# Kernel tuning notes

Measured on AMD Instinct MI355X. Metric: run time of the kernel, lower is better.

## Reference

```python
import jax, jax.numpy as jnp
import numpy as np

NUM_EXPERTS = 8
TOP_K = 2
HIDDEN = 1024
NUM_TOKENS = 8192


def setup_inputs() -> dict:
    key = jax.random.key(0)
    k1, k2, k3 = jax.random.split(key, 3)
    x = jax.random.normal(k1, (NUM_TOKENS, HIDDEN), dtype=jnp.float32)
    # gate: nn.Linear(hidden, num_experts, bias=False) -> weight [E, H]
    gate_w = jax.random.normal(k2, (NUM_EXPERTS, HIDDEN), dtype=jnp.float32) * 0.02
    # experts: nn.Linear(hidden, hidden, bias=False) stacked -> [E, H_out, H_in]
    expert_w = jax.random.normal(k3, (NUM_EXPERTS, HIDDEN, HIDDEN), dtype=jnp.float32) * 0.02
    return {"x": x, "gate_w": gate_w, "expert_w": expert_w}


def reference(x, gate_w, expert_w):
    # --- routing ---
    logits = jnp.einsum("th,eh->te", x, gate_w)          # [T, E]
    probs = jax.nn.softmax(logits, axis=-1)
    weights, indices = jax.lax.top_k(probs, TOP_K)        # [T, K], [T, K]

    # --- expert compute (equivalent of dispatch + per-expert GEMM) ---
    # y_e = x @ W_e^T for every expert; tokens then gather their top-k rows.
    all_y = jnp.einsum("td,ehd->eth", x, expert_w)        # [E, T, H]

    # --- weighted combine (gather by routed expert ids) ---
    t_idx = jnp.arange(x.shape[0])[None, :]               # [1, T]
    y_sel = all_y[indices.T, t_idx, :]                    # [K, T, H]
    out = jnp.einsum("tk,kth->th", weights, y_sel)        # [T, H]
    return out
```

## Files before the change

### kernel.cpp

```cpp
#include <hip/hip_runtime.h>
#include <hip/hip_bf16.h>
#include <stdint.h>

#define NUM_TOKENS 8192
#define HIDDEN 1024
#define NEXP 8
#define TOPK 2

typedef __bf16 bf16;
typedef __bf16 bf16x4 __attribute__((ext_vector_type(4)));
typedef __bf16 bf16x8 __attribute__((ext_vector_type(8)));
typedef float f32x4 __attribute__((ext_vector_type(4)));

__device__ __forceinline__ void gld_lds16(const void* g, void* l) {
  __builtin_amdgcn_global_load_lds(
      (const __attribute__((address_space(1))) void*)(uintptr_t)g,
      (__attribute__((address_space(3))) void*)(uint32_t)(uintptr_t)l,
      16, 0, 0);
}

__global__ __launch_bounds__(256) void gate_route_kernel(
    const float* __restrict__ x, const float* __restrict__ gw,
    bf16* __restrict__ xbf, int* __restrict__ echoice, float* __restrict__ pchoice)
{
  const int wid  = threadIdx.x >> 6;
  const int lane = threadIdx.x & 63;
  const int t = blockIdx.x * 4 + wid;

  const float* xrow = x + (size_t)t * HIDDEN;
  bf16* xbrow = xbf + (size_t)t * HIDDEN;

  float acc[NEXP];
#pragma unroll
  for (int e = 0; e < NEXP; ++e) acc[e] = 0.f;

#pragma unroll
  for (int it = 0; it < 4; ++it) {
    const int idx = it * 256 + lane * 4;
    float4 xv = *(const float4*)(xrow + idx);
    bf16x4 xb;
    xb[0] = (bf16)xv.x; xb[1] = (bf16)xv.y; xb[2] = (bf16)xv.z; xb[3] = (bf16)xv.w;
    *(bf16x4*)(xbrow + idx) = xb;
#pragma unroll
    for (int e = 0; e < NEXP; ++e) {
      float4 gv = *(const float4*)(gw + e * HIDDEN + idx);
      acc[e] += xv.x * gv.x + xv.y * gv.y + xv.z * gv.z + xv.w * gv.w;
    }
  }
#pragma unroll
  for (int e = 0; e < NEXP; ++e) {
#pragma unroll
    for (int off = 32; off > 0; off >>= 1)
      acc[e] += __shfl_xor(acc[e], off, 64);
  }

  if (lane == 0) {
    float m = acc[0];
#pragma unroll
    for (int e = 1; e < NEXP; ++e) m = fmaxf(m, acc[e]);
    float p[NEXP]; float s = 0.f;
#pragma unroll
    for (int e = 0; e < NEXP; ++e) { p[e] = expf(acc[e] - m); s += p[e]; }
    const float inv = 1.f / s;
#pragma unroll
    for (int e = 0; e < NEXP; ++e) p[e] *= inv;
    int i0 = 0; float p0 = p[0];
#pragma unroll
    for (int e = 1; e < NEXP; ++e) if (p[e] > p0) { p0 = p[e]; i0 = e; }
    int i1 = -1; float p1 = -1.f;
#pragma unroll
    for (int e = 0; e < NEXP; ++e) if (e != i0 && p[e] > p1) { p1 = p[e]; i1 = e; }

    echoice[t]              = i0;
    echoice[NUM_TOKENS + t] = i1;
    pchoice[t]              = p0;
    pchoice[NUM_TOKENS + t] = p1;
  }
}

__global__ __launch_bounds__(1024) void build_lists_kernel(
    const int* __restrict__ echoice, const float* __restrict__ pchoice,
    int* __restrict__ cnt, int* __restrict__ tok, float* __restrict__ wt)
{
  const int tid  = threadIdx.x;
  const int wave = tid >> 6;
  const int lane = tid & 63;
  const int k = wave >> 3;
  const int w = wave & 7;
  const int tbase = w * 1024;

  const int*   ec = echoice + k * NUM_TOKENS;
  const float* pc = pchoice + k * NUM_TOKENS;

  __shared__ int wcnt[2][8][NEXP];
  __shared__ int woff[2][8][NEXP];

  const unsigned long long lower = ((unsigned long long)1 << lane) - 1;

  int   ev[16];
  float pv[16];
#pragma unroll
  for (int c = 0; c < 16; ++c) {
    ev[c] = ec[tbase + c * 64 + lane];
    pv[c] = pc[tbase + c * 64 + lane];
  }

  int cl[NEXP];
#pragma unroll
  for (int e = 0; e < NEXP; ++e) cl[e] = 0;
#pragma unroll
  for (int c = 0; c < 16; ++c) {
#pragma unroll
    for (int l = 0; l < NEXP; ++l)
      cl[l] += __popcll(__ballot(ev[c] == l));
  }
  if (lane < NEXP) wcnt[k][w][lane] = cl[lane];
  __syncthreads();

  if (lane < NEXP) {
    int off = 0;
#pragma unroll
    for (int ww = 0; ww < 8; ++ww) {
      if (ww == w) woff[k][w][lane] = off;
      off += wcnt[k][ww][lane];
    }
    if (w == 0) cnt[k * NEXP + lane] = off;
  }
  __syncthreads();

  int run[NEXP];
#pragma unroll
  for (int e = 0; e < NEXP; ++e) run[e] = woff[k][w][e];
#pragma unroll
  for (int c = 0; c < 16; ++c) {
    const int e = ev[c];
    int pos = 0;
#pragma unroll
    for (int l = 0; l < NEXP; ++l) {
      const unsigned long long m = __ballot(ev[c] == l);
      if (e == l) pos = run[l] + __popcll(m & lower);
      run[l] += __popcll(m);
    }
    const int list = k * NEXP + e;
    tok[(size_t)list * NUM_TOKENS + pos] = tbase + c * 64 + lane;
    wt [(size_t)list * NUM_TOKENS + pos] = pv[c];
  }
}

__global__ __launch_bounds__(256) void convert_w_kernel(
    const float* __restrict__ w, bf16* __restrict__ wbf)
{
  const size_t i = ((size_t)blockIdx.x * 256 + threadIdx.x) * 4;
  float4 v = *(const float4*)(w + i);
  bf16x4 b;
  b[0] = (bf16)v.x; b[1] = (bf16)v.y; b[2] = (bf16)v.z; b[3] = (bf16)v.w;
  *(bf16x4*)(wbf + i) = b;
}

__global__ __launch_bounds__(256) void moe_gemm_kernel(
    const bf16* __restrict__ xbf, const bf16* __restrict__ wbf,
    const int* __restrict__ cnt, const int* __restrict__ tok,
    const float* __restrict__ wt, float* __restrict__ out)
{
  const int e  = blockIdx.z >> 1;
  const int k  = blockIdx.z & 1;
  const int list = k * NEXP + e;
  const int mt = blockIdx.y;
  const int nt = blockIdx.x;
  const int count = cnt[list];
  const int m0 = mt * 128;
  if (m0 >= count) return;
  const int rows = min(128, count - m0);

  __shared__ __align__(16) bf16 As[128 * 32];
  __shared__ __align__(16) bf16 Bs[128 * 32];
  __shared__ int   tok_s[128];
  __shared__ float wt_s[128];

  const int tid = threadIdx.x;
  if (tid < 128) {
    if (tid < rows) {
      tok_s[tid] = tok[(size_t)list * NUM_TOKENS + m0 + tid];
      wt_s[tid]  = wt [(size_t)list * NUM_TOKENS + m0 + tid];
    } else { tok_s[tid] = 0; wt_s[tid] = 0.f; }
  }
  __syncthreads();

  const int rr = tid >> 2;
  const int c8 = tid & 3;
  const bf16* gA0 = xbf + (size_t)tok_s[rr] * HIDDEN + c8 * 8;
  const bf16* gA1 = xbf + (size_t)tok_s[64 + rr] * HIDDEN + c8 * 8;
  const bf16* gB0 = wbf + (size_t)e * HIDDEN * HIDDEN
                  + (size_t)(nt * 128 + rr) * HIDDEN + c8 * 8;
  const bf16* gB1 = gB0 + (size_t)64 * HIDDEN;
  bf16* lA = As + tid * 8;
  bf16* lB = Bs + tid * 8;

  const int wid  = tid >> 6;
  const int lane = tid & 63;
  const int wm = (wid >> 1) * 64;
  const int wn = (wid & 1) * 64;
  const int qm = lane & 15;
  const int q8 = (lane >> 4) * 8;

  f32x4 acc[4][4];
#pragma unroll
  for (int i = 0; i < 4; ++i)
#pragma unroll
    for (int j = 0; j < 4; ++j) acc[i][j] = (f32x4){0.f, 0.f, 0.f, 0.f};

  for (int kc = 0; kc < HIDDEN; kc += 32) {
    gld_lds16(gA0 + kc, lA);
    gld_lds16(gA1 + kc, lA + 64 * 32);
    gld_lds16(gB0 + kc, lB);
    gld_lds16(gB1 + kc, lB + 64 * 32);
    __syncthreads();

    bf16x8 a[4], b[4];
#pragma unroll
    for (int i = 0; i < 4; ++i)
      a[i] = *(const bf16x8*)(As + (wm + i * 16 + qm) * 32 + q8);
#pragma unroll
    for (int j = 0; j < 4; ++j)
      b[j] = *(const bf16x8*)(Bs + (wn + j * 16 + qm) * 32 + q8);
#pragma unroll
    for (int i = 0; i < 4; ++i)
#pragma unroll
      for (int j = 0; j < 4; ++j)
        acc[i][j] = __builtin_amdgcn_mfma_f32_16x16x32_bf16(a[i], b[j], acc[i][j], 0, 0, 0);
    __syncthreads();
  }

  const int h0 = nt * 128 + wn + (lane & 15);
#pragma unroll
  for (int i = 0; i < 4; ++i) {
    const int rbase = wm + i * 16 + (lane >> 4) * 4;
#pragma unroll
    for (int r = 0; r < 4; ++r) {
      const int rl = rbase + r;
      if (rl < rows) {
        const int t = tok_s[rl];
        const float w = wt_s[rl];
        float* orow = out + (size_t)t * HIDDEN + h0;
#pragma unroll
        for (int j = 0; j < 4; ++j) {
          const float v = w * acc[i][j][r];
          unsafeAtomicAdd(orow + j * 16, v);
        }
      }
    }
  }
}

extern "C" void kernel_launch(void* const* d_in, const int* in_sizes, int n_in,
                              void* d_out, int out_size, void* d_ws, size_t ws_size,
                              hipStream_t stream) {
  const float* x  = (const float*)d_in[0];
  const float* gw = (const float*)d_in[1];
  const float* ew = (const float*)d_in[2];
  float* out = (float*)d_out;

  char* ws = (char*)d_ws;
  int*   cnt     = (int*)ws;
  int*   echoice = (int*)(ws + 256);
  float* pchoice = (float*)(ws + 256 + (size_t)2 * NUM_TOKENS * 4);
  int*   tok = (int*)(ws + 256 + (size_t)4 * NUM_TOKENS * 4);
  float* wt  = (float*)(ws + 256 + (size_t)20 * NUM_TOKENS * 4);
  bf16*  xbf = (bf16*)(ws + 256 + (size_t)36 * NUM_TOKENS * 4);
  bf16*  wbf = (bf16*)((char*)xbf + (size_t)NUM_TOKENS * HIDDEN * 2);

  hipMemsetAsync(out, 0, (size_t)NUM_TOKENS * HIDDEN * sizeof(float), stream);

  gate_route_kernel<<<NUM_TOKENS / 4, 256, 0, stream>>>(x, gw, xbf, echoice, pchoice);
  build_lists_kernel<<<1, 1024, 0, stream>>>(echoice, pchoice, cnt, tok, wt);
  convert_w_kernel<<<(NEXP * HIDDEN * HIDDEN) / (4 * 256), 256, 0, stream>>>(ew, wbf);

  dim3 grid(HIDDEN / 128, NUM_TOKENS / 128, 2 * NEXP);
  moe_gemm_kernel<<<grid, 256, 0, stream>>>(xbf, wbf, cnt, tok, wt, out);
}
```

Baseline: 233.0 us.

## Double-buffer MoE GEMM with K=64 swizzled LDS tiles and parallelize list building

```diff
diff --git a/kernel.cpp b/kernel.cpp
--- a/kernel.cpp
+++ b/kernel.cpp
@@ -82,68 +82,51 @@
     const int* __restrict__ echoice, const float* __restrict__ pchoice,
     int* __restrict__ cnt, int* __restrict__ tok, float* __restrict__ wt)
 {
+  const int list = blockIdx.x;
+  const int k = list >> 3;
+  const int e = list & 7;
   const int tid  = threadIdx.x;
   const int wave = tid >> 6;
   const int lane = tid & 63;
-  const int k = wave >> 3;
-  const int w = wave & 7;
-  const int tbase = w * 1024;
+  const int tbase = wave * 512;
 
   const int*   ec = echoice + k * NUM_TOKENS;
   const float* pc = pchoice + k * NUM_TOKENS;
 
-  __shared__ int wcnt[2][8][NEXP];
-  __shared__ int woff[2][8][NEXP];
+  __shared__ int wcnt[16];
+  __shared__ int woff[16];
 
   const unsigned long long lower = ((unsigned long long)1 << lane) - 1;
 
-  int   ev[16];
-  float pv[16];
-#pragma unroll
-  for (int c = 0; c < 16; ++c) {
+  int   ev[8];
+  float pv[8];
+#pragma unroll
+  for (int c = 0; c < 8; ++c) {
     ev[c] = ec[tbase + c * 64 + lane];
     pv[c] = pc[tbase + c * 64 + lane];
   }
-
-  int cl[NEXP];
-#pragma unroll
-  for (int e = 0; e < NEXP; ++e) cl[e] = 0;
-#pragma unroll
-  for (int c = 0; c < 16; ++c) {
-#pragma unroll
-    for (int l = 0; l < NEXP; ++l)
-      cl[l] += __popcll(__ballot(ev[c] == l));
-  }
-  if (lane < NEXP) wcnt[k][w][lane] = cl[lane];
-  __syncthreads();
-
-  if (lane < NEXP) {
+  unsigned long long m[8];
+  int cl = 0;
+#pragma unroll
+  for (int c = 0; c < 8; ++c) { m[c] = __ballot(ev[c] == e); cl += __popcll(m[c]); }
+  if (lane == 0) wcnt[wave] = cl;
+  __syncthreads();
+  if (tid == 0) {
     int off = 0;
 #pragma unroll
-    for (int ww = 0; ww < 8; ++ww) {
-      if (ww == w) woff[k][w][lane] = off;
-      off += wcnt[k][ww][lane];
-    }
-    if (w == 0) cnt[k * NEXP + lane] = off;
-  }
-  __syncthreads();
-
-  int run[NEXP];
-#pragma unroll
-  for (int e = 0; e < NEXP; ++e) run[e] = woff[k][w][e];
-#pragma unroll
-  for (int c = 0; c < 16; ++c) {
-    const int e = ev[c];
-    int pos = 0;
-#pragma unroll
-    for (int l = 0; l < NEXP; ++l) {
-      const unsigned long long m = __ballot(ev[c] == l);
-      if (e == l) pos = run[l] + __popcll(m & lower);
-      run[l] += __popcll(m);
-    }
-    const int list = k * NEXP + e;
-    tok[(size_t)list * NUM_TOKENS + pos] = tbase + c * 64 + lane;
-    wt [(size_t)list * NUM_TOKENS + pos] = pv[c];
+    for (int w = 0; w < 16; ++w) { woff[w] = off; off += wcnt[w]; }
+    cnt[list] = off;
+  }
+  __syncthreads();
+  int run = woff[wave];
+#pragma unroll
+  for (int c = 0; c < 8; ++c) {
+    if (ev[c] == e) {
+      const int pos = run + __popcll(m[c] & lower);
+      tok[(size_t)list * NUM_TOKENS + pos] = tbase + c * 64 + lane;
+      wt [(size_t)list * NUM_TOKENS + pos] = pv[c];
+    }
+    run += __popcll(m[c]);
   }
 }
 
@@ -172,8 +155,8 @@
   if (m0 >= count) return;
   const int rows = min(128, count - m0);
 
-  __shared__ __align__(16) bf16 As[128 * 32];
-  __shared__ __align__(16) bf16 Bs[128 * 32];
+  __shared__ __align__(16) bf16 As[2 * 128 * 64];
+  __shared__ __align__(16) bf16 Bs[2 * 128 * 64];
   __shared__ int   tok_s[128];
   __shared__ float wt_s[128];
 
@@ -186,22 +169,25 @@
   }
   __syncthreads();
 
-  const int rr = tid >> 2;
-  const int c8 = tid & 3;
-  const bf16* gA0 = xbf + (size_t)tok_s[rr] * HIDDEN + c8 * 8;
-  const bf16* gA1 = xbf + (size_t)tok_s[64 + rr] * HIDDEN + c8 * 8;
-  const bf16* gB0 = wbf + (size_t)e * HIDDEN * HIDDEN
-                  + (size_t)(nt * 128 + rr) * HIDDEN + c8 * 8;
-  const bf16* gB1 = gB0 + (size_t)64 * HIDDEN;
-  bf16* lA = As + tid * 8;
-  bf16* lB = Bs + tid * 8;
+  const int csrc = (tid & 7) ^ ((tid >> 3) & 7);
+  const bf16* aptr[4];
+  const bf16* bptr[4];
+  const size_t eoff = (size_t)e * HIDDEN * HIDDEN;
+#pragma unroll
+  for (int p = 0; p < 4; ++p) {
+    const int r = p * 32 + (tid >> 3);
+    aptr[p] = xbf + (size_t)tok_s[r] * HIDDEN + csrc * 8;
+    bptr[p] = wbf + eoff + (size_t)(nt * 128 + r) * HIDDEN + csrc * 8;
+  }
+  bf16* la = As + tid * 8;
+  bf16* lb = Bs + tid * 8;
 
   const int wid  = tid >> 6;
   const int lane = tid & 63;
   const int wm = (wid >> 1) * 64;
   const int wn = (wid & 1) * 64;
   const int qm = lane & 15;
-  const int q8 = (lane >> 4) * 8;
+  const int l4 = lane >> 4;
 
   f32x4 acc[4][4];
 #pragma unroll
@@ -209,26 +195,52 @@
 #pragma unroll
     for (int j = 0; j < 4; ++j) acc[i][j] = (f32x4){0.f, 0.f, 0.f, 0.f};
 
-  for (int kc = 0; kc < HIDDEN; kc += 32) {
-    gld_lds16(gA0 + kc, lA);
-    gld_lds16(gA1 + kc, lA + 64 * 32);
-    gld_lds16(gB0 + kc, lB);
-    gld_lds16(gB1 + kc, lB + 64 * 32);
-    __syncthreads();
-
-    bf16x8 a[4], b[4];
-#pragma unroll
-    for (int i = 0; i < 4; ++i)
-      a[i] = *(const bf16x8*)(As + (wm + i * 16 + qm) * 32 + q8);
-#pragma unroll
-    for (int j = 0; j < 4; ++j)
-      b[j] = *(const bf16x8*)(Bs + (wn + j * 16 + qm) * 32 + q8);
-#pragma unroll
-    for (int i = 0; i < 4; ++i)
-#pragma unroll
-      for (int j = 0; j < 4; ++j)
-        acc[i][j] = __builtin_amdgcn_mfma_f32_16x16x32_bf16(a[i], b[j], acc[i][j], 0, 0, 0);
-    __syncthreads();
+#pragma unroll
+  for (int p = 0; p < 4; ++p) {
+    gld_lds16(aptr[p], la + p * 2048);
+    gld_lds16(bptr[p], lb + p * 2048);
+  }
+  __syncthreads();
+
+  for (int t = 0; t < 16; ++t) {
+    const int cur = t & 1;
+    if (t < 15) {
+      const int kc = (t + 1) * 64;
+      bf16* lan = la + (cur ^ 1) * 8192;
+      bf16* lbn = lb + (cur ^ 1) * 8192;
+#pragma unroll
+      for (int p = 0; p < 4; ++p) {
+        gld_lds16(aptr[p] + kc, lan + p * 2048);
+        gld_lds16(bptr[p] + kc, lbn + p * 2048);
+      }
+    }
+
+    const bf16* Ab = As + cur * 8192;
+    const bf16* Bb = Bs + cur * 8192;
+    bf16x8 a[4][2], b[4][2];
+#pragma unroll
+    for (int i = 0; i < 4; ++i) {
+      const int r = wm + i * 16 + qm;
+      const int x7 = r & 7;
+      a[i][0] = *(const bf16x8*)(Ab + r * 64 + (l4 ^ x7) * 8);
+      a[i][1] = *(const bf16x8*)(Ab + r * 64 + ((4 + l4) ^ x7) * 8);
+    }
+#pragma unroll
+    for (int j = 0; j < 4; ++j) {
+      const int r = wn + j * 16 + qm;
+      const int x7 = r & 7;
+      b[j][0] = *(const bf16x8*)(Bb + r * 64 + (l4 ^ x7) * 8);
+      b[j][1] = *(const bf16x8*)(Bb + r * 64 + ((4 + l4) ^ x7) * 8);
+    }
+#pragma unroll
+    for (int h = 0; h < 2; ++h)
+#pragma unroll
+      for (int i = 0; i < 4; ++i)
+#pragma unroll
+        for (int j = 0; j < 4; ++j)
+          acc[i][j] = __builtin_amdgcn_mfma_f32_16x16x32_bf16(a[i][h], b[j][h], acc[i][j], 0, 0, 0);
+
+    if (t < 15) __syncthreads();
   }
 
   const int h0 = nt * 128 + wn + (lane & 15);
@@ -272,7 +284,7 @@
   hipMemsetAsync(out, 0, (size_t)NUM_TOKENS * HIDDEN * sizeof(float), stream);
 
   gate_route_kernel<<<NUM_TOKENS / 4, 256, 0, stream>>>(x, gw, xbf, echoice, pchoice);
-  build_lists_kernel<<<1, 1024, 0, stream>>>(echoice, pchoice, cnt, tok, wt);
+  build_lists_kernel<<<2 * NEXP, 1024, 0, stream>>>(echoice, pchoice, cnt, tok, wt);
   convert_w_kernel<<<(NEXP * HIDDEN * HIDDEN) / (4 * 256), 256, 0, stream>>>(ew, wbf);
 
   dim3 grid(HIDDEN / 128, NUM_TOKENS / 128, 2 * NEXP);
```

Measured after the change: 210.1 us. -9.8%, faster.
